# Kernel tuning notes

Hardware: AMD Instinct MI355X
Metric: run time of the kernel (lower is better)

Reference implementation:

```python
import jax, jax.numpy as jnp
import numpy as np


def setup_inputs() -> dict:
    key = jax.random.key(0)
    k1, k2, k3, k4 = jax.random.split(key, 4)
    d_in, d_out, B, T = 1024, 1024, 4, 2048
    scale = 1.0 / np.sqrt(d_in)
    return {
        "x": jax.random.normal(k1, (B, T, d_in), dtype=jnp.float32),
        "Wq": jax.random.normal(k2, (d_in, d_out), dtype=jnp.float32) * scale,
        "Wk": jax.random.normal(k3, (d_in, d_out), dtype=jnp.float32) * scale,
        "Wv": jax.random.normal(k4, (d_in, d_out), dtype=jnp.float32) * scale,
    }


def reference(x, Wq, Wk, Wv):
    # x: [B, T, d_in]; Wq/Wk/Wv: [d_in, d_out] (Linear, bias=False)
    q = jnp.einsum("btd,de->bte", x, Wq)
    k = jnp.einsum("btd,de->bte", x, Wk)
    v = jnp.einsum("btd,de->bte", x, Wv)
    d_out = k.shape[-1]
    scores = jnp.einsum("bqe,bke->bqk", q, k)  # [B, T, T]
    T = x.shape[1]
    causal = jnp.triu(jnp.ones((T, T), dtype=bool), k=1)  # True above diagonal
    scores = jnp.where(causal[None, :, :], -jnp.inf, scores)
    # original divides after masking; -inf stays -inf so math is identical
    att = jax.nn.softmax(scores / jnp.sqrt(jnp.asarray(d_out, scores.dtype)), axis=-1)
    # dropout p=0.0 -> identity
    return jnp.einsum("bqk,bke->bqe", att, v)
```

## Files before the change

kernel.cpp:

```cpp
#include <hip/hip_runtime.h>
#include <stdint.h>
#include <math.h>

typedef unsigned short u16;
typedef __bf16 bf16x8 __attribute__((ext_vector_type(8)));
typedef float f32x4 __attribute__((ext_vector_type(4)));

enum { M_SCORE = 1, M_PV = 2 };

__device__ __forceinline__ u16 f2bf(float f) {
    union { float f; unsigned int u; } a; a.f = f;
    unsigned int u = a.u;
    u += 0x7FFFu + ((u >> 16) & 1u);
    return (u16)(u >> 16);
}

__device__ __forceinline__ void async_load16(const void* g, void* l) {
    __builtin_amdgcn_global_load_lds(
        (const __attribute__((address_space(1))) void*)g,
        (__attribute__((address_space(3))) void*)l,
        16, 0, 0);
}

template<int MODE, int TBM>
__device__ __forceinline__ void gemm_core(
    const u16* __restrict__ A, const u16* __restrict__ Bt,
    void* __restrict__ Cv, float* __restrict__ rowsum,
    int bm, int bn, int bz, int M, int N, int K, float kfac,
    u16* As, u16* Bs)
{
    constexpr int KB  = 64;
    constexpr int NI  = TBM / 32;
    constexpr int ACH = TBM / 32;
    constexpr int BCH = 4;

    const int tid  = threadIdx.x;
    const int lane = tid & 63;
    const int wv   = tid >> 6;
    const int wm   = wv >> 1;
    const int wn   = wv & 1;

    f32x4 acc[NI][4] = {};

    const int rowA0 = bm * TBM, rowB0 = bn * 128;
    const int lrow  = lane >> 3;
    const int lslot = lane & 7;
    const int sg    = (lslot ^ lrow) * 8;

    int kEnd = K;
    if (MODE == M_PV) { int ke = (bm + 1) * TBM; kEnd = ke < K ? ke : K; }

    const int lm   = lane & 15;
    const int quad = lane >> 4;
    const int rx   = lm & 7;

    for (int k0 = 0; k0 < kEnd; k0 += KB) {
        #pragma unroll
        for (int c = 0; c < ACH; ++c) {
            const int cc  = wv * ACH + c;
            const int row = cc * 8 + lrow;
            const u16* src;
            if (MODE == M_PV)
                src = &A[(size_t)(k0 >> 7) * 16384
                         + (size_t)((rowA0 & 127) + row) * 128 + (k0 & 127) + sg];
            else
                src = &A[(size_t)(rowA0 + row) * K + k0 + sg];
            async_load16(src, &As[cc * 512 + lane * 8]);
        }
        #pragma unroll
        for (int c = 0; c < BCH; ++c) {
            const int cc  = wv * BCH + c;
            const int row = cc * 8 + lrow;
            async_load16(&Bt[(size_t)(rowB0 + row) * K + k0 + sg], &Bs[cc * 512 + lane * 8]);
        }
        __syncthreads();

        #pragma unroll
        for (int h = 0; h < 2; ++h) {
            const int sl = (((h * 4 + quad) ^ rx) * 8);
            bf16x8 af[NI], bfr[4];
            #pragma unroll
            for (int i = 0; i < NI; ++i)
                af[i] = *reinterpret_cast<const bf16x8*>(
                    &As[(wm * (TBM / 2) + i * 16 + lm) * KB + sl]);
            #pragma unroll
            for (int j = 0; j < 4; ++j)
                bfr[j] = *reinterpret_cast<const bf16x8*>(
                    &Bs[(wn * 64 + j * 16 + lm) * KB + sl]);
            #pragma unroll
            for (int i = 0; i < NI; ++i)
                #pragma unroll
                for (int j = 0; j < 4; ++j)
                    acc[i][j] = __builtin_amdgcn_mfma_f32_16x16x32_bf16(af[i], bfr[j], acc[i][j], 0, 0, 0);
        }
        __syncthreads();
    }

    if (MODE == M_SCORE) {
        u16* E = (u16*)Cv;
        const int rbase = rowA0 & 127;
        float rs[NI][4];
        #pragma unroll
        for (int i = 0; i < NI; ++i)
            #pragma unroll
            for (int g = 0; g < 4; ++g) rs[i][g] = 0.f;
        #pragma unroll
        for (int i = 0; i < NI; ++i)
            #pragma unroll
            for (int j = 0; j < 4; ++j) {
                const int rl = wm * (TBM / 2) + i * 16 + quad * 4;
                const int cl = wn * 64 + j * 16 + lm;
                const int c  = rowB0 + cl;
                #pragma unroll
                for (int g = 0; g < 4; ++g) {
                    const int r = rowA0 + rl + g;
                    float e = (c <= r) ? exp2f(acc[i][j][g] * kfac) : 0.f;
                    E[(size_t)(rbase + rl + g) * 128 + cl] = f2bf(e);
                    rs[i][g] += e;
                }
            }
        #pragma unroll
        for (int i = 0; i < NI; ++i)
            #pragma unroll
            for (int g = 0; g < 4; ++g) {
                float v = rs[i][g];
                v += __shfl_xor(v, 1); v += __shfl_xor(v, 2);
                v += __shfl_xor(v, 4); v += __shfl_xor(v, 8);
                rs[i][g] = v;
            }
        if (lm == 0) {
            #pragma unroll
            for (int i = 0; i < NI; ++i)
                #pragma unroll
                for (int g = 0; g < 4; ++g) {
                    const int r = rowA0 + wm * (TBM / 2) + i * 16 + quad * 4 + g;
                    atomicAdd(&rowsum[(size_t)bz * M + r], rs[i][g]);
                }
        }
    } else {
        float* C = (float*)Cv + (size_t)bz * ((size_t)M * N);
        #pragma unroll
        for (int i = 0; i < NI; ++i) {
            const int r0 = rowA0 + wm * (TBM / 2) + i * 16 + quad * 4;
            float inv[4];
            #pragma unroll
            for (int g = 0; g < 4; ++g)
                inv[g] = 1.f / rowsum[(size_t)bz * M + r0 + g];
            #pragma unroll
            for (int j = 0; j < 4; ++j) {
                const int c0 = rowB0 + wn * 64 + j * 16 + lm;
                #pragma unroll
                for (int g = 0; g < 4; ++g)
                    C[(size_t)(r0 + g) * N + c0] = acc[i][j][g] * inv[g];
            }
        }
    }
}

__global__ __launch_bounds__(512, 2)
void k_qkv2(const u16* __restrict__ Xb, const u16* __restrict__ Wt,
            u16* __restrict__ Q, int M, int N, int K)
{
    extern __shared__ __attribute__((aligned(16))) u16 S[];
    const int tid  = threadIdx.x;
    const int lane = tid & 63;
    const int wv   = tid >> 6;
    const int wm   = wv >> 2;
    const int wn   = wv & 3;
    const int bn   = blockIdx.x;
    const int bm   = blockIdx.y;
    const int rowA0 = bm * 128, rowB0 = bn * 256;

    const int lrow  = lane >> 3;
    const int lslot = lane & 7;
    const int sg    = (lslot ^ lrow) * 8;
    const int lm    = lane & 15;
    const int quad  = lane >> 4;
    const int rx    = lm & 7;

    f32x4 acc[4][4] = {};

    const int nt = K >> 6;

    auto stage = [&](int t, int b) {
        u16* As = S + b * 24576;
        u16* Bs = As + 8192;
        const int k0 = t << 6;
        #pragma unroll
        for (int c = 0; c < 2; ++c) {
            const int cc  = wv * 2 + c;
            const int row = cc * 8 + lrow;
            async_load16(&Xb[(size_t)(rowA0 + row) * K + k0 + sg], &As[cc * 512 + lane * 8]);
        }
        #pragma unroll
        for (int c = 0; c < 4; ++c) {
            const int cc  = wv * 4 + c;
            const int row = cc * 8 + lrow;
            async_load16(&Wt[(size_t)(rowB0 + row) * K + k0 + sg], &Bs[cc * 512 + lane * 8]);
        }
    };

    auto compute = [&](int b) {
        const u16* As = S + b * 24576;
        const u16* Bs = As + 8192;
        #pragma unroll
        for (int h = 0; h < 2; ++h) {
            const int sl = (((h * 4 + quad) ^ rx) * 8);
            bf16x8 af[4], bfr[4];
            #pragma unroll
            for (int i = 0; i < 4; ++i)
                af[i] = *reinterpret_cast<const bf16x8*>(
                    &As[(wm * 64 + i * 16 + lm) * 64 + sl]);
            #pragma unroll
            for (int j = 0; j < 4; ++j)
                bfr[j] = *reinterpret_cast<const bf16x8*>(
                    &Bs[(wn * 64 + j * 16 + lm) * 64 + sl]);
            #pragma unroll
            for (int i = 0; i < 4; ++i)
                #pragma unroll
                for (int j = 0; j < 4; ++j)
                    acc[i][j] = __builtin_amdgcn_mfma_f32_16x16x32_bf16(af[i], bfr[j], acc[i][j], 0, 0, 0);
        }
    };

    stage(0, 0);
    stage(1, 1);
    asm volatile("s_waitcnt vmcnt(6)" ::: "memory");
    __builtin_amdgcn_s_barrier();

    int cb = 0;
    #pragma unroll 1
    for (int t = 0; t < nt - 2; ++t) {
        int sb = cb + 2; if (sb >= 3) sb -= 3;
        stage(t + 2, sb);
        compute(cb);
        asm volatile("s_waitcnt vmcnt(6)" ::: "memory");
        __builtin_amdgcn_s_barrier();
        if (++cb == 3) cb = 0;
    }
    compute(cb);
    asm volatile("s_waitcnt vmcnt(0)" ::: "memory");
    __builtin_amdgcn_s_barrier();
    if (++cb == 3) cb = 0;
    compute(cb);

    u16* C = Q + (size_t)(bn >> 2) * ((size_t)M * 1024);
    const int cbase = (rowB0 & 1023) + wn * 64;
    #pragma unroll
    for (int i = 0; i < 4; ++i)
        #pragma unroll
        for (int j = 0; j < 4; ++j) {
            const int r0 = rowA0 + wm * 64 + i * 16 + quad * 4;
            const int c0 = cbase + j * 16 + lm;
            #pragma unroll
            for (int g = 0; g < 4; ++g)
                C[(size_t)(r0 + g) * 1024 + c0] = f2bf(acc[i][j][g]);
        }
}

__global__ __launch_bounds__(256)
void k_score_vt(const u16* __restrict__ Q, const u16* __restrict__ Kb,
                u16* __restrict__ Epk, float* __restrict__ rowsum,
                const u16* __restrict__ Vb, u16* __restrict__ Vt,
                int T, int D, float kfac, int nTri)
{
    __shared__ __attribute__((aligned(16))) u16 As[64 * 64];
    __shared__ __attribute__((aligned(16))) u16 Bs[128 * 64];
    __shared__ u16 tt[32][33];
    const int bz = blockIdx.z;

    if ((int)blockIdx.x < nTri) {
        const int idx = blockIdx.x;
        int w = (int)sqrtf((float)idx + 0.5f);
        while (w * w > idx) --w;
        while ((w + 1) * (w + 1) <= idx) ++w;
        int bm, bn;
        if (idx < w * w + w) { bm = 2 * w - 1; bn = idx - w * w; }
        else                 { bm = 2 * w;     bn = idx - (w * w + w); }
        const int bm128 = bm >> 1;
        const int tile  = bm128 * (bm128 + 1) / 2 + bn;
        u16* Etile = Epk + ((size_t)bz * 136 + tile) * 16384;
        gemm_core<M_SCORE, 64>(Q + (size_t)bz * T * D, Kb + (size_t)bz * T * D,
                               Etile, rowsum, bm, bn, bz, T, T, D, kfac, As, Bs);
    } else {
        const int t  = blockIdx.x - nTri;
        const int cx = t & 31;
        const int cy = t >> 5;
        const u16* V = Vb + (size_t)bz * T * D;
        u16*      Vo = Vt + (size_t)bz * D * T;
        const int c0 = cx * 32, r0 = cy * 32;
        const int tx = threadIdx.x & 31, ty = threadIdx.x >> 5;
        #pragma unroll
        for (int s = 0; s < 32; s += 8)
            tt[ty + s][tx] = V[(size_t)(r0 + ty + s) * D + c0 + tx];
        __syncthreads();
        #pragma unroll
        for (int s = 0; s < 32; s += 8)
            Vo[(size_t)(c0 + ty + s) * T + r0 + tx] = tt[tx][ty + s];
    }
}

__global__ __launch_bounds__(256)
void k_pv(const u16* __restrict__ Epk, const u16* __restrict__ Vt,
          float* __restrict__ out, const float* __restrict__ rowsum,
          int T, int D)
{
    __shared__ __attribute__((aligned(16))) u16 As[64 * 64];
    __shared__ __attribute__((aligned(16))) u16 Bs[128 * 64];
    const int bz = blockIdx.z;
    const int bm = (gridDim.y - 1) - blockIdx.y;
    const int bm128 = bm >> 1;
    const u16* Arow = Epk + ((size_t)bz * 136 + (size_t)bm128 * (bm128 + 1) / 2) * 16384;
    gemm_core<M_PV, 64>(Arow, Vt + (size_t)bz * D * T,
                        out, (float*)rowsum, bm, blockIdx.x, bz,
                        T, D, T, 0.f, As, Bs);
}

__global__ __launch_bounds__(256)
void k_prep(const float* __restrict__ x,
            const float* __restrict__ W0, const float* __restrict__ W1,
            const float* __restrict__ W2,
            u16* __restrict__ Xb, u16* __restrict__ Wt, float* __restrict__ RS,
            int D, int nCX, int nW)
{
    const int bx = blockIdx.x;
    if (bx < nCX) {
        long long i = ((long long)bx * 256 + threadIdx.x) * 8;
        const float4 a = *(const float4*)(x + i);
        const float4 b = *(const float4*)(x + i + 4);
        union { u16 u[8]; float4 v; } r;
        r.u[0] = f2bf(a.x); r.u[1] = f2bf(a.y); r.u[2] = f2bf(a.z); r.u[3] = f2bf(a.w);
        r.u[4] = f2bf(b.x); r.u[5] = f2bf(b.y); r.u[6] = f2bf(b.z); r.u[7] = f2bf(b.w);
        *(float4*)(Xb + i) = r.v;
    } else if (bx < nCX + nW) {
        __shared__ u16 t[32][33];
        const int w  = bx - nCX;
        const int z  = w >> 10;
        const int rm = w & 1023;
        const float* W = z == 0 ? W0 : (z == 1 ? W1 : W2);
        u16* dst = Wt + (size_t)z * D * D;
        const int c0 = (rm & 31) * 32, r0 = (rm >> 5) * 32;
        const int tx = threadIdx.x & 31, ty = threadIdx.x >> 5;
        #pragma unroll
        for (int s = 0; s < 32; s += 8)
            t[ty + s][tx] = f2bf(W[(size_t)(r0 + ty + s) * D + c0 + tx]);
        __syncthreads();
        #pragma unroll
        for (int s = 0; s < 32; s += 8)
            dst[(size_t)(c0 + ty + s) * D + r0 + tx] = t[tx][ty + s];
    } else {
        const int t = bx - nCX - nW;
        ((float4*)RS)[t * 256 + threadIdx.x] = float4{0.f, 0.f, 0.f, 0.f};
    }
}

extern "C" void kernel_launch(void* const* d_in, const int* in_sizes, int n_in,
                              void* d_out, int out_size, void* d_ws, size_t ws_size,
                              hipStream_t stream)
{
    const int B = 4, T = 2048, D = 1024;
    const float* x  = (const float*)d_in[0];
    const float* Wq = (const float*)d_in[1];
    const float* Wk = (const float*)d_in[2];
    const float* Wv = (const float*)d_in[3];
    float* out = (float*)d_out;

    const size_t nX = (size_t)B * T * D;
    u16* Xb  = (u16*)d_ws;
    u16* Wt  = Xb + nX;
    u16* Epk = (u16*)d_ws;
    u16* Q   = Wt + 3 * (size_t)D * D;
    u16* Kb  = Q + nX;
    u16* Vb  = Kb + nX;
    u16* Vt  = Vb + nX;
    float* RS = (float*)(Vt + nX);

    const float kfac = 1.4426950408889634f / 32.0f;
    const int nTri64 = 272;
    const int nCX = (int)(nX / (8 * 256));
    const int nW  = 3 * (D / 32) * (D / 32);
    const int nRS = (B * T) / (4 * 256);

    static bool attr_done = false;
    if (!attr_done) {
        (void)hipFuncSetAttribute((const void*)k_qkv2,
                                  hipFuncAttributeMaxDynamicSharedMemorySize,
                                  147456);
        attr_done = true;
    }

    k_prep<<<dim3(nCX + nW + nRS), 256, 0, stream>>>(
        x, Wq, Wk, Wv, Xb, Wt, RS, D, nCX, nW);
    k_qkv2<<<dim3(3 * D / 256, (B * T) / 128), 512, 147456, stream>>>(
        Xb, Wt, Q, B * T, 3 * D, D);
    k_score_vt<<<dim3(nTri64 + (D / 32) * (T / 32), 1, B), 256, 0, stream>>>(
        Q, Kb, Epk, RS, Vb, Vt, T, D, kfac, nTri64);
    k_pv<<<dim3(D / 128, T / 64, B), 256, 0, stream>>>(
        Epk, Vt, out, RS, T, D);
}
```

Before: 233.5 us.

## Store E and V in MFMA fragment order so PV loads operands directly

The score kernel now stages each wave's exp tile in a swizzled LDS patch and writes it to global memory in MFMA fragment-packed layout. The V transpose writes V in the same fragment-packed layout. The PV kernel is rewritten to load bf16x8 fragments straight from global memory with one coalesced 16-byte load per lane, with no LDS staging and no __syncthreads. This removes LDS round trips and barriers in PV, at the cost of relying on cache for operand reuse across waves and losing explicit prefetch/pipelining.

```diff
diff --git a/kernel.cpp b/kernel.cpp
--- a/kernel.cpp
+++ b/kernel.cpp
@@ -5,8 +5,6 @@
 typedef unsigned short u16;
 typedef __bf16 bf16x8 __attribute__((ext_vector_type(8)));
 typedef float f32x4 __attribute__((ext_vector_type(4)));
-
-enum { M_SCORE = 1, M_PV = 2 };
 
 __device__ __forceinline__ u16 f2bf(float f) {
     union { float f; unsigned int u; } a; a.f = f;
@@ -22,54 +20,41 @@
         16, 0, 0);
 }
 
-template<int MODE, int TBM>
-__device__ __forceinline__ void gemm_core(
+
+__device__ __forceinline__ void gemm_score(
     const u16* __restrict__ A, const u16* __restrict__ Bt,
-    void* __restrict__ Cv, float* __restrict__ rowsum,
-    int bm, int bn, int bz, int M, int N, int K, float kfac,
+    u16* __restrict__ Etile, float* __restrict__ rowsum,
+    int bm, int bn, int bz, int M, int K, float kfac,
     u16* As, u16* Bs)
 {
-    constexpr int KB  = 64;
-    constexpr int NI  = TBM / 32;
-    constexpr int ACH = TBM / 32;
-    constexpr int BCH = 4;
-
+    constexpr int KB = 64;
     const int tid  = threadIdx.x;
     const int lane = tid & 63;
     const int wv   = tid >> 6;
     const int wm   = wv >> 1;
     const int wn   = wv & 1;
 
-    f32x4 acc[NI][4] = {};
-
-    const int rowA0 = bm * TBM, rowB0 = bn * 128;
+    f32x4 acc[2][4] = {};
+
+    const int rowA0 = bm * 64, rowB0 = bn * 128;
     const int lrow  = lane >> 3;
     const int lslot = lane & 7;
     const int sg    = (lslot ^ lrow) * 8;
 
-    int kEnd = K;
-    if (MODE == M_PV) { int ke = (bm + 1) * TBM; kEnd = ke < K ? ke : K; }
-
     const int lm   = lane & 15;
     const int quad = lane >> 4;
     const int rx   = lm & 7;
 
-    for (int k0 = 0; k0 < kEnd; k0 += KB) {
-        #pragma unroll
-        for (int c = 0; c < ACH; ++c) {
-            const int cc  = wv * ACH + c;
+    for (int k0 = 0; k0 < K; k0 += KB) {
+        #pragma unroll
+        for (int c = 0; c < 2; ++c) {
+            const int cc  = wv * 2 + c;
             const int row = cc * 8 + lrow;
-            const u16* src;
-            if (MODE == M_PV)
-                src = &A[(size_t)(k0 >> 7) * 16384
-                         + (size_t)((rowA0 & 127) + row) * 128 + (k0 & 127) + sg];
-            else
-                src = &A[(size_t)(rowA0 + row) * K + k0 + sg];
-            async_load16(src, &As[cc * 512 + lane * 8]);
-        }
-        #pragma unroll
-        for (int c = 0; c < BCH; ++c) {
-            const int cc  = wv * BCH + c;
+            async_load16(&A[(size_t)(rowA0 + row) * K + k0 + sg], &As[cc * 512 + lane * 8]);
+        }
+        #pragma unroll
+        for (int c = 0; c < 4; ++c) {
+            const int cc  = wv * 4 + c;
             const int row = cc * 8 + lrow;
             async_load16(&Bt[(size_t)(rowB0 + row) * K + k0 + sg], &Bs[cc * 512 + lane * 8]);
         }
@@ -78,17 +63,17 @@
         #pragma unroll
         for (int h = 0; h < 2; ++h) {
             const int sl = (((h * 4 + quad) ^ rx) * 8);
-            bf16x8 af[NI], bfr[4];
-            #pragma unroll
-            for (int i = 0; i < NI; ++i)
+            bf16x8 af[2], bfr[4];
+            #pragma unroll
+            for (int i = 0; i < 2; ++i)
                 af[i] = *reinterpret_cast<const bf16x8*>(
-                    &As[(wm * (TBM / 2) + i * 16 + lm) * KB + sl]);
+                    &As[(wm * 32 + i * 16 + lm) * KB + sl]);
             #pragma unroll
             for (int j = 0; j < 4; ++j)
                 bfr[j] = *reinterpret_cast<const bf16x8*>(
                     &Bs[(wn * 64 + j * 16 + lm) * KB + sl]);
             #pragma unroll
-            for (int i = 0; i < NI; ++i)
+            for (int i = 0; i < 2; ++i)
                 #pragma unroll
                 for (int j = 0; j < 4; ++j)
                     acc[i][j] = __builtin_amdgcn_mfma_f32_16x16x32_bf16(af[i], bfr[j], acc[i][j], 0, 0, 0);
@@ -96,65 +81,56 @@
         __syncthreads();
     }
 
-    if (MODE == M_SCORE) {
-        u16* E = (u16*)Cv;
-        const int rbase = rowA0 & 127;
-        float rs[NI][4];
-        #pragma unroll
-        for (int i = 0; i < NI; ++i)
-            #pragma unroll
-            for (int g = 0; g < 4; ++g) rs[i][g] = 0.f;
-        #pragma unroll
-        for (int i = 0; i < NI; ++i)
-            #pragma unroll
-            for (int j = 0; j < 4; ++j) {
-                const int rl = wm * (TBM / 2) + i * 16 + quad * 4;
-                const int cl = wn * 64 + j * 16 + lm;
-                const int c  = rowB0 + cl;
-                #pragma unroll
-                for (int g = 0; g < 4; ++g) {
-                    const int r = rowA0 + rl + g;
-                    float e = (c <= r) ? exp2f(acc[i][j][g] * kfac) : 0.f;
-                    E[(size_t)(rbase + rl + g) * 128 + cl] = f2bf(e);
-                    rs[i][g] += e;
-                }
+    u16* patch = Bs + wv * 2048;
+    float rs[2][4];
+    #pragma unroll
+    for (int i = 0; i < 2; ++i)
+        #pragma unroll
+        for (int g = 0; g < 4; ++g) rs[i][g] = 0.f;
+    #pragma unroll
+    for (int i = 0; i < 2; ++i)
+        #pragma unroll
+        for (int j = 0; j < 4; ++j) {
+            const int cl = j * 16 + lm;
+            const int c  = rowB0 + wn * 64 + cl;
+            #pragma unroll
+            for (int g = 0; g < 4; ++g) {
+                const int rl = i * 16 + quad * 4 + g;
+                const int r  = rowA0 + wm * 32 + rl;
+                float e = (c <= r) ? exp2f(acc[i][j][g] * kfac) : 0.f;
+                patch[rl * 64 + (cl ^ ((rl & 7) << 3))] = f2bf(e);
+                rs[i][g] += e;
             }
-        #pragma unroll
-        for (int i = 0; i < NI; ++i)
+        }
+    #pragma unroll
+    for (int i = 0; i < 2; ++i)
+        #pragma unroll
+        for (int g = 0; g < 4; ++g) {
+            float v = rs[i][g];
+            v += __shfl_xor(v, 1); v += __shfl_xor(v, 2);
+            v += __shfl_xor(v, 4); v += __shfl_xor(v, 8);
+            rs[i][g] = v;
+        }
+    if (lm == 0) {
+        #pragma unroll
+        for (int i = 0; i < 2; ++i)
             #pragma unroll
             for (int g = 0; g < 4; ++g) {
-                float v = rs[i][g];
-                v += __shfl_xor(v, 1); v += __shfl_xor(v, 2);
-                v += __shfl_xor(v, 4); v += __shfl_xor(v, 8);
-                rs[i][g] = v;
+                const int r = rowA0 + wm * 32 + i * 16 + quad * 4 + g;
+                atomicAdd(&rowsum[(size_t)bz * M + r], rs[i][g]);
             }
-        if (lm == 0) {
-            #pragma unroll
-            for (int i = 0; i < NI; ++i)
-                #pragma unroll
-                for (int g = 0; g < 4; ++g) {
-                    const int r = rowA0 + wm * (TBM / 2) + i * 16 + quad * 4 + g;
-                    atomicAdd(&rowsum[(size_t)bz * M + r], rs[i][g]);
-                }
-        }
-    } else {
-        float* C = (float*)Cv + (size_t)bz * ((size_t)M * N);
-        #pragma unroll
-        for (int i = 0; i < NI; ++i) {
-            const int r0 = rowA0 + wm * (TBM / 2) + i * 16 + quad * 4;
-            float inv[4];
-            #pragma unroll
-            for (int g = 0; g < 4; ++g)
-                inv[g] = 1.f / rowsum[(size_t)bz * M + r0 + g];
-            #pragma unroll
-            for (int j = 0; j < 4; ++j) {
-                const int c0 = rowB0 + wn * 64 + j * 16 + lm;
-                #pragma unroll
-                for (int g = 0; g < 4; ++g)
-                    C[(size_t)(r0 + g) * N + c0] = acc[i][j][g] * inv[g];
-            }
-        }
-    }
+    }
+    const int r16b = ((rowA0 & 127) >> 4) + wm * 2;
+    #pragma unroll
+    for (int i2 = 0; i2 < 2; ++i2)
+        #pragma unroll
+        for (int kk = 0; kk < 2; ++kk) {
+            const int row_l = i2 * 16 + lm;
+            const int colsw = (kk * 32 + quad * 8) ^ (rx << 3);
+            bf16x8 v = *reinterpret_cast<const bf16x8*>(&patch[row_l * 64 + colsw]);
+            *reinterpret_cast<bf16x8*>(
+                &Etile[(size_t)((((r16b + i2) << 2) + wn * 2 + kk) << 9) + lane * 8]) = v;
+        }
 }
 
 __global__ __launch_bounds__(512, 2)
@@ -179,7 +155,6 @@
     const int rx    = lm & 7;
 
     f32x4 acc[4][4] = {};
-
     const int nt = K >> 6;
 
     auto stage = [&](int t, int b) {
@@ -261,7 +236,7 @@
 __global__ __launch_bounds__(256)
 void k_score_vt(const u16* __restrict__ Q, const u16* __restrict__ Kb,
                 u16* __restrict__ Epk, float* __restrict__ rowsum,
-                const u16* __restrict__ Vb, u16* __restrict__ Vt,
+                const u16* __restrict__ Vb, u16* __restrict__ Vf,
                 int T, int D, float kfac, int nTri)
 {
     __shared__ __attribute__((aligned(16))) u16 As[64 * 64];
@@ -280,40 +255,100 @@
         const int bm128 = bm >> 1;
         const int tile  = bm128 * (bm128 + 1) / 2 + bn;
         u16* Etile = Epk + ((size_t)bz * 136 + tile) * 16384;
-        gemm_core<M_SCORE, 64>(Q + (size_t)bz * T * D, Kb + (size_t)bz * T * D,
-                               Etile, rowsum, bm, bn, bz, T, T, D, kfac, As, Bs);
+        gemm_score(Q + (size_t)bz * T * D, Kb + (size_t)bz * T * D,
+                   Etile, rowsum, bm, bn, bz, T, D, kfac, As, Bs);
     } else {
         const int t  = blockIdx.x - nTri;
         const int cx = t & 31;
         const int cy = t >> 5;
         const u16* V = Vb + (size_t)bz * T * D;
-        u16*      Vo = Vt + (size_t)bz * D * T;
+        u16*      Vo = Vf + (size_t)bz * ((size_t)D * T);
         const int c0 = cx * 32, r0 = cy * 32;
         const int tx = threadIdx.x & 31, ty = threadIdx.x >> 5;
         #pragma unroll
         for (int s = 0; s < 32; s += 8)
             tt[ty + s][tx] = V[(size_t)(r0 + ty + s) * D + c0 + tx];
         __syncthreads();
-        #pragma unroll
-        for (int s = 0; s < 32; s += 8)
-            Vo[(size_t)(c0 + ty + s) * T + r0 + tx] = tt[tx][ty + s];
+        if (threadIdx.x < 128) {
+            const int l  = threadIdx.x & 63;
+            const int f  = threadIdx.x >> 6;
+            const int dl = f * 16 + (l & 15);
+            const int tb = (l >> 4) * 8;
+            union { u16 u[8]; float4 v; } r;
+            #pragma unroll
+            for (int e = 0; e < 8; ++e) r.u[e] = tt[tb + e][dl];
+            const int d16g = cx * 2 + f;
+            *reinterpret_cast<float4*>(
+                &Vo[(size_t)((d16g * (T / 32) + cy) << 9) + l * 8]) = r.v;
+        }
     }
 }
 
 __global__ __launch_bounds__(256)
-void k_pv(const u16* __restrict__ Epk, const u16* __restrict__ Vt,
-          float* __restrict__ out, const float* __restrict__ rowsum,
-          int T, int D)
-{
-    __shared__ __attribute__((aligned(16))) u16 As[64 * 64];
-    __shared__ __attribute__((aligned(16))) u16 Bs[128 * 64];
-    const int bz = blockIdx.z;
-    const int bm = (gridDim.y - 1) - blockIdx.y;
+void k_pv2(const u16* __restrict__ Epk, const u16* __restrict__ Vf,
+           float* __restrict__ out, const float* __restrict__ rowsum,
+           int T, int D)
+{
+    const int bz   = blockIdx.z;
+    const int bm   = (gridDim.y - 1) - blockIdx.y;
+    const int bn   = blockIdx.x;
+    const int tid  = threadIdx.x;
+    const int lane = tid & 63;
+    const int wv   = tid >> 6;
+    const int wm   = wv >> 1;
+    const int wn   = wv & 1;
+    const int lm   = lane & 15;
+    const int quad = lane >> 4;
+
     const int bm128 = bm >> 1;
-    const u16* Arow = Epk + ((size_t)bz * 136 + (size_t)bm128 * (bm128 + 1) / 2) * 16384;
-    gemm_core<M_PV, 64>(Arow, Vt + (size_t)bz * D * T,
-                        out, (float*)rowsum, bm, blockIdx.x, bz,
-                        T, D, T, 0.f, As, Bs);
+    const u16* Etri = Epk + ((size_t)bz * 136 + (size_t)bm128 * (bm128 + 1) / 2) * 16384;
+    const int r16b  = ((bm & 1) << 2) + wm * 2;
+    const int kEnd  = (bm + 1) * 64;
+    const u16* vfb  = Vf + (size_t)bz * ((size_t)D * T);
+    const int  TS   = T >> 5;
+
+    f32x4 acc[2][4] = {};
+
+    #pragma unroll 2
+    for (int k0 = 0; k0 < kEnd; k0 += 32) {
+        const u16* tb = Etri + (size_t)(k0 >> 7) * 16384;
+        const int  kk = (k0 >> 5) & 3;
+        const int  kt = k0 >> 5;
+        bf16x8 af[2], bf[4];
+        #pragma unroll
+        for (int i = 0; i < 2; ++i)
+            af[i] = *reinterpret_cast<const bf16x8*>(
+                &tb[(size_t)(((((r16b + i) << 2) + kk)) << 9) + lane * 8]);
+        #pragma unroll
+        for (int j = 0; j < 4; ++j) {
+            const int d16 = (bn << 3) + (wn << 2) + j;
+            bf[j] = *reinterpret_cast<const bf16x8*>(
+                &vfb[(size_t)((d16 * TS + kt) << 9) + lane * 8]);
+        }
+        #pragma unroll
+        for (int i = 0; i < 2; ++i)
+            #pragma unroll
+            for (int j = 0; j < 4; ++j)
+                acc[i][j] = __builtin_amdgcn_mfma_f32_16x16x32_bf16(af[i], bf[j], acc[i][j], 0, 0, 0);
+    }
+
+    const int rowA0 = bm * 64;
+    float* C = out + (size_t)bz * ((size_t)T * D);
+    #pragma unroll
+    for (int i = 0; i < 2; ++i) {
+        const int r0 = rowA0 + wm * 32 + i * 16 + quad * 4;
+        float inv[4];
+        #pragma unroll
+        for (int g = 0; g < 4; ++g)
+            inv[g] = 1.f / rowsum[(size_t)bz * T + r0 + g];
+        #pragma unroll
+        for (int j = 0; j < 4; ++j) {
+            const int c0 = (bn << 7) + wn * 64 + j * 16 + lm;
+            #pragma unroll
+            for (int g = 0; g < 4; ++g)
+                C[(size_t)(r0 + g) * D + c0] = acc[i][j][g] * inv[g];
+        }
+    }
 }
 
 __global__ __launch_bounds__(256)
@@ -372,8 +407,8 @@
     u16* Q   = Wt + 3 * (size_t)D * D;
     u16* Kb  = Q + nX;
     u16* Vb  = Kb + nX;
-    u16* Vt  = Vb + nX;
-    float* RS = (float*)(Vt + nX);
+    u16* Vf  = Vb + nX;
+    float* RS = (float*)(Vf + nX);
 
     const float kfac = 1.4426950408889634f / 32.0f;
     const int nTri64 = 272;
@@ -394,7 +429,7 @@
     k_qkv2<<<dim3(3 * D / 256, (B * T) / 128), 512, 147456, stream>>>(
         Xb, Wt, Q, B * T, 3 * D, D);
     k_score_vt<<<dim3(nTri64 + (D / 32) * (T / 32), 1, B), 256, 0, stream>>>(
-        Q, Kb, Epk, RS, Vb, Vt, T, D, kfac, nTri64);
-    k_pv<<<dim3(D / 128, T / 64, B), 256, 0, stream>>>(
-        Epk, Vt, out, RS, T, D);
-}
+        Q, Kb, Epk, RS, Vb, Vf, T, D, kfac, nTri64);
+    k_pv2<<<dim3(D / 128, T / 64, B), 256, 0, stream>>>(
+        Epk, Vf, out, RS, T, D);
+}
```

Result: slower. 260.7 us (+11.6%).

## Fuse V transpose into QKV GEMM epilogue via shared-memory staging

Applied to the files above, without the earlier changes.

The V projection blocks of the QKV GEMM now write their output already transposed into Vt. The tile is staged through shared memory and stored with 16-byte vectors, so the separate transpose blocks in the score kernel are no longer launched. This removes a full write and re-read of V plus a poorly coalesced 2-byte transpose. The cost is an extra shared-memory round trip and two barriers in the epilogue of a third of the GEMM blocks.

```diff
diff --git a/kernel.cpp b/kernel.cpp
--- a/kernel.cpp
+++ b/kernel.cpp
@@ -159,7 +159,7 @@
 
 __global__ __launch_bounds__(512, 2)
 void k_qkv2(const u16* __restrict__ Xb, const u16* __restrict__ Wt,
-            u16* __restrict__ Q, int M, int N, int K)
+            u16* __restrict__ Q, u16* __restrict__ Vt, int M, int N, int K)
 {
     extern __shared__ __attribute__((aligned(16))) u16 S[];
     const int tid  = threadIdx.x;
@@ -179,7 +179,6 @@
     const int rx    = lm & 7;
 
     f32x4 acc[4][4] = {};
-
     const int nt = K >> 6;
 
     auto stage = [&](int t, int b) {
@@ -244,60 +243,69 @@
     if (++cb == 3) cb = 0;
     compute(cb);
 
-    u16* C = Q + (size_t)(bn >> 2) * ((size_t)M * 1024);
-    const int cbase = (rowB0 & 1023) + wn * 64;
-    #pragma unroll
-    for (int i = 0; i < 4; ++i)
-        #pragma unroll
-        for (int j = 0; j < 4; ++j) {
-            const int r0 = rowA0 + wm * 64 + i * 16 + quad * 4;
-            const int c0 = cbase + j * 16 + lm;
-            #pragma unroll
-            for (int g = 0; g < 4; ++g)
-                C[(size_t)(r0 + g) * 1024 + c0] = f2bf(acc[i][j][g]);
-        }
+    if (bn < 8) {
+        u16* C = Q + (size_t)(bn >> 2) * ((size_t)M * 1024);
+        const int cbase = (rowB0 & 1023) + wn * 64;
+        #pragma unroll
+        for (int i = 0; i < 4; ++i)
+            #pragma unroll
+            for (int j = 0; j < 4; ++j) {
+                const int r0 = rowA0 + wm * 64 + i * 16 + quad * 4;
+                const int c0 = cbase + j * 16 + lm;
+                #pragma unroll
+                for (int g = 0; g < 4; ++g)
+                    C[(size_t)(r0 + g) * 1024 + c0] = f2bf(acc[i][j][g]);
+            }
+    } else {
+        __syncthreads();
+        #pragma unroll
+        for (int i = 0; i < 4; ++i)
+            #pragma unroll
+            for (int j = 0; j < 4; ++j) {
+                const int d_l = wn * 64 + j * 16 + lm;
+                const int t_l = wm * 64 + i * 16 + quad * 4;
+                union { u16 u[4]; uint2 v; } p;
+                #pragma unroll
+                for (int g = 0; g < 4; ++g) p.u[g] = f2bf(acc[i][j][g]);
+                *reinterpret_cast<uint2*>(&S[d_l * 136 + t_l]) = p.v;
+            }
+        __syncthreads();
+        const int bzv  = rowA0 >> 11;
+        const int t0   = rowA0 & 2047;
+        const int dbs  = (bn & 3) * 256;
+        u16* Vo = Vt + (size_t)bzv * (1024u * 2048u);
+        #pragma unroll
+        for (int it = 0; it < 8; ++it) {
+            const int d_l = it * 32 + (tid >> 4);
+            const int tp  = (tid & 15) * 8;
+            bf16x8 v = *reinterpret_cast<const bf16x8*>(&S[d_l * 136 + tp]);
+            *reinterpret_cast<bf16x8*>(
+                &Vo[(size_t)(dbs + d_l) * 2048 + t0 + tp]) = v;
+        }
+    }
 }
 
 __global__ __launch_bounds__(256)
 void k_score_vt(const u16* __restrict__ Q, const u16* __restrict__ Kb,
                 u16* __restrict__ Epk, float* __restrict__ rowsum,
-                const u16* __restrict__ Vb, u16* __restrict__ Vt,
-                int T, int D, float kfac, int nTri)
+                int T, int D, float kfac)
 {
     __shared__ __attribute__((aligned(16))) u16 As[64 * 64];
     __shared__ __attribute__((aligned(16))) u16 Bs[128 * 64];
-    __shared__ u16 tt[32][33];
     const int bz = blockIdx.z;
 
-    if ((int)blockIdx.x < nTri) {
-        const int idx = blockIdx.x;
-        int w = (int)sqrtf((float)idx + 0.5f);
-        while (w * w > idx) --w;
-        while ((w + 1) * (w + 1) <= idx) ++w;
-        int bm, bn;
-        if (idx < w * w + w) { bm = 2 * w - 1; bn = idx - w * w; }
-        else                 { bm = 2 * w;     bn = idx - (w * w + w); }
-        const int bm128 = bm >> 1;
-        const int tile  = bm128 * (bm128 + 1) / 2 + bn;
-        u16* Etile = Epk + ((size_t)bz * 136 + tile) * 16384;
-        gemm_core<M_SCORE, 64>(Q + (size_t)bz * T * D, Kb + (size_t)bz * T * D,
-                               Etile, rowsum, bm, bn, bz, T, T, D, kfac, As, Bs);
-    } else {
-        const int t  = blockIdx.x - nTri;
-        const int cx = t & 31;
-        const int cy = t >> 5;
-        const u16* V = Vb + (size_t)bz * T * D;
-        u16*      Vo = Vt + (size_t)bz * D * T;
-        const int c0 = cx * 32, r0 = cy * 32;
-        const int tx = threadIdx.x & 31, ty = threadIdx.x >> 5;
-        #pragma unroll
-        for (int s = 0; s < 32; s += 8)
-            tt[ty + s][tx] = V[(size_t)(r0 + ty + s) * D + c0 + tx];
-        __syncthreads();
-        #pragma unroll
-        for (int s = 0; s < 32; s += 8)
-            Vo[(size_t)(c0 + ty + s) * T + r0 + tx] = tt[tx][ty + s];
-    }
+    const int idx = blockIdx.x;
+    int w = (int)sqrtf((float)idx + 0.5f);
+    while (w * w > idx) --w;
+    while ((w + 1) * (w + 1) <= idx) ++w;
+    int bm, bn;
+    if (idx < w * w + w) { bm = 2 * w - 1; bn = idx - w * w; }
+    else                 { bm = 2 * w;     bn = idx - (w * w + w); }
+    const int bm128 = bm >> 1;
+    const int tile  = bm128 * (bm128 + 1) / 2 + bn;
+    u16* Etile = Epk + ((size_t)bz * 136 + tile) * 16384;
+    gemm_core<M_SCORE, 64>(Q + (size_t)bz * T * D, Kb + (size_t)bz * T * D,
+                           Etile, rowsum, bm, bn, bz, T, T, D, kfac, As, Bs);
 }
 
 __global__ __launch_bounds__(256)
@@ -392,9 +400,9 @@
     k_prep<<<dim3(nCX + nW + nRS), 256, 0, stream>>>(
         x, Wq, Wk, Wv, Xb, Wt, RS, D, nCX, nW);
     k_qkv2<<<dim3(3 * D / 256, (B * T) / 128), 512, 147456, stream>>>(
-        Xb, Wt, Q, B * T, 3 * D, D);
-    k_score_vt<<<dim3(nTri64 + (D / 32) * (T / 32), 1, B), 256, 0, stream>>>(
-        Q, Kb, Epk, RS, Vb, Vt, T, D, kfac, nTri64);
+        Xb, Wt, Q, Vt, B * T, 3 * D, D);
+    k_score_vt<<<dim3(nTri64, 1, B), 256, 0, stream>>>(
+        Q, Kb, Epk, RS, T, D, kfac);
     k_pv<<<dim3(D / 128, T / 64, B), 256, 0, stream>>>(
         Epk, Vt, out, RS, T, D);
 }
```

Result: slower. 238.8 us (+2.2%).
